# Performance work log

Hardware: AMD Instinct MI355X
Metric: run time of the kernel (lower is better)

The kernel has to match this reference:

```python
import jax, jax.numpy as jnp
import numpy as np

D_IN, H, L, B, ALPHA = 42, 800, 256, 16, 20
BOND_LENS = jnp.array([145.801, 152.326, 132.868], dtype=jnp.float32)  # N-CA, CA-C, C-N (pm)
BOND_ANGS = jnp.array([2.124, 1.941, 2.028], dtype=jnp.float32)


def setup_inputs() -> dict:
    key = jax.random.key(0)
    ks = jax.random.split(key, 10)
    s = 0.05
    return {
        "x": jax.random.normal(ks[0], (B, L, D_IN), dtype=jnp.float32),
        "w_ih_l0": jax.random.normal(ks[1], (2, 4 * H, D_IN), dtype=jnp.float32) * s,
        "w_hh_l0": jax.random.normal(ks[2], (2, 4 * H, H), dtype=jnp.float32) * s,
        "b_l0": jax.random.normal(ks[3], (2, 4 * H), dtype=jnp.float32) * s,
        "w_ih_l1": jax.random.normal(ks[4], (2, 4 * H, 2 * H), dtype=jnp.float32) * s,
        "w_hh_l1": jax.random.normal(ks[5], (2, 4 * H, H), dtype=jnp.float32) * s,
        "b_l1": jax.random.normal(ks[6], (2, 4 * H), dtype=jnp.float32) * s,
        "w_lin": jax.random.normal(ks[7], (ALPHA, 2 * H), dtype=jnp.float32) * s,
        "b_lin": jax.random.normal(ks[8], (ALPHA,), dtype=jnp.float32) * s,
        "alphabet": jax.random.uniform(ks[9], (ALPHA, 3), dtype=jnp.float32,
                                       minval=-np.pi, maxval=np.pi),
    }


def _lstm_dir(xs, w_ih, w_hh, b, reverse):
    # xs: (L, B, in) -> (L, B, H); PyTorch gate order i,f,g,o
    bsz = xs.shape[1]
    hdim = w_hh.shape[1]
    def step(carry, x_t):
        hp, cp = carry
        g = x_t @ w_ih.T + hp @ w_hh.T + b
        i, f, gg, o = jnp.split(g, 4, axis=-1)
        c = jax.nn.sigmoid(f) * cp + jax.nn.sigmoid(i) * jnp.tanh(gg)
        hn = jax.nn.sigmoid(o) * jnp.tanh(c)
        return (hn, c), hn
    init = (jnp.zeros((bsz, hdim), xs.dtype), jnp.zeros((bsz, hdim), xs.dtype))
    _, ys = jax.lax.scan(step, init, xs, reverse=reverse)
    return ys


def _bilstm_layer(xs, w_ih, w_hh, b):
    fwd = _lstm_dir(xs, w_ih[0], w_hh[0], b[0], reverse=False)
    bwd = _lstm_dir(xs, w_ih[1], w_hh[1], b[1], reverse=True)
    return jnp.concatenate([fwd, bwd], axis=-1)  # (L, B, 2H)


def _calculate_coordinates(torsions):
    # torsions: (L, B, 3) dihedrals -> NeRF backbone extension, (3 + 3L, B, 3)
    bsz = torsions.shape[1]
    A0 = jnp.broadcast_to(jnp.array([0., 0., 1.], jnp.float32), (bsz, 3))
    B0 = jnp.broadcast_to(jnp.array([0., 1., 0.], jnp.float32), (bsz, 3))
    C0 = jnp.broadcast_to(jnp.array([1., 0., 0.], jnp.float32), (bsz, 3))

    def step(carry, tors):
        A_, B_, C_ = carry
        outs = []
        for i in range(3):  # place N, CA, C of next residue
            T, R, P = BOND_ANGS[i], BOND_LENS[i], tors[:, i]
            D2 = jnp.stack([-R * jnp.cos(T) * jnp.ones_like(P),
                            R * jnp.cos(P) * jnp.sin(T),
                            R * jnp.sin(P) * jnp.sin(T)], axis=1)  # (B,3)
            bc = (C_ - B_) / jnp.linalg.norm(C_ - B_, axis=1, keepdims=True)
            Nv = jnp.cross(B_ - A_, bc)
            n = Nv / jnp.linalg.norm(Nv, axis=1, keepdims=True)
            M = jnp.stack([bc, jnp.cross(n, bc), n], axis=2)  # (B,3,3)
            D = jnp.einsum('bij,bj->bi', M, D2) + C_
            outs.append(D)
            A_, B_, C_ = B_, C_, D
        return (A_, B_, C_), jnp.stack(outs)  # (3, B, 3)

    _, new = jax.lax.scan(step, (A0, B0, C0), torsions)  # (L, 3, B, 3)
    init = jnp.stack([A0, B0, C0])  # (3, B, 3)
    return jnp.concatenate([init, new.reshape(-1, bsz, 3)], axis=0)


def reference(x, w_ih_l0, w_hh_l0, b_l0, w_ih_l1, w_hh_l1, b_l1, w_lin, b_lin, alphabet):
    xs = jnp.transpose(x, (1, 0, 2))  # (L, B, d_in), matches torch transpose(0,1)
    h1 = _bilstm_layer(xs, w_ih_l0, w_hh_l0, b_l0)
    h2 = _bilstm_layer(h1, w_ih_l1, w_hh_l1, b_l1)  # (L, B, 2H); eval mode: no dropout
    # Angularization: linear -> softmax over alphabet -> weighted dihedral lookup
    probs = jax.nn.softmax(h2 @ w_lin.T + b_lin, axis=-1)  # (L, B, ALPHA)
    sin_a, cos_a = jnp.sin(alphabet), jnp.cos(alphabet)     # (ALPHA, 3)
    ang = jnp.arctan2(probs @ sin_a, probs @ cos_a)         # (L, B, 3)
    return _calculate_coordinates(ang)
```

## Files before the change

kernel.cpp:

```cpp
#include <hip/hip_runtime.h>
#include <stdint.h>

typedef __attribute__((ext_vector_type(8))) short short8;
typedef __attribute__((ext_vector_type(4))) float floatx4;
typedef __attribute__((ext_vector_type(4))) unsigned int uintx4;

#define DEVINL __device__ __forceinline__

DEVINL unsigned short f2bf(float f) {
    unsigned int u = __float_as_uint(f);
    u += 0x7FFFu + ((u >> 16) & 1u);
    return (unsigned short)(u >> 16);
}
DEVINL float bf2f(unsigned short h) {
    return __uint_as_float(((unsigned int)h) << 16);
}
DEVINL float sigf(float x)     { return 1.0f / (1.0f + __expf(-x)); }
DEVINL float tanhfast(float x) { return 2.0f / (1.0f + __expf(-2.0f * x)) - 1.0f; }

constexpr int L_SEQ = 256, BATCH = 16, HID = 800, NGATE = 3200, DIN = 42, NALPHA = 20;
constexpr int HSLOT = BATCH * HID;
constexpr int NBLK_SCAN = 200;

constexpr size_t OFF_FLAGS   = 0;
constexpr size_t SZ_FLAGS    = 131072;
constexpr size_t SZ_WHH_L    = 10240000;
constexpr size_t OFF_WHH_HI  = SZ_FLAGS;
constexpr size_t OFF_WHH_LO  = OFF_WHH_HI + 2 * SZ_WHH_L;
constexpr size_t SZ_WIH1     = 20480000;
constexpr size_t OFF_WIH1_HI = OFF_WHH_LO + 2 * SZ_WHH_L;
constexpr size_t OFF_WIH1_LO = OFF_WIH1_HI + SZ_WIH1;
constexpr size_t OFF_PRE     = OFF_WIH1_LO + SZ_WIH1;
constexpr size_t SZ_PRE      = (size_t)2 * L_SEQ * BATCH * NGATE * 4;
constexpr size_t SZ_HP       = (size_t)257 * HSLOT * 4;
constexpr size_t OFF_H       = OFF_PRE + SZ_PRE;
constexpr size_t OFF_ANG     = OFF_H + 4 * SZ_HP;

__global__ __launch_bounds__(256) void pack_whh_kernel(
    const float* __restrict__ w0, const float* __restrict__ w1,
    unsigned short* __restrict__ hi, unsigned short* __restrict__ lo)
{
    size_t g = (size_t)blockIdx.x * 256 + threadIdx.x;
    if (g >= 1280000) return;
    int l = (int)(g & 63);
    size_t gg = g >> 6;
    int kk = (int)(gg % 25); gg /= 25;
    int nt = (int)(gg % 2);  gg /= 2;
    int jc = (int)(gg % 100); gg /= 100;
    int d  = (int)(gg % 2);
    int layer = (int)(gg / 2);
    const float* W = layer ? w1 : w0;
    int lr = nt * 16 + (l & 15);
    int gate = lr >> 3, jj = lr & 7;
    int r  = gate * 800 + jc * 8 + jj;
    int k0 = kk * 32 + (l >> 4) * 8;
    const float* s = W + ((size_t)d * NGATE + r) * HID + k0;
    short8 vh, vl;
    #pragma unroll
    for (int j = 0; j < 8; ++j) {
        float w = s[j];
        unsigned short h = f2bf(w);
        vh[j] = (short)h;
        vl[j] = (short)f2bf(w - bf2f(h));
    }
    size_t idx = (size_t)layer * 640000 + ((size_t)d * 100 + jc) * 3200
               + (size_t)(nt * 25 + kk) * 64 + l;
    ((short8*)hi)[idx] = vh;
    ((short8*)lo)[idx] = vl;
}

__global__ __launch_bounds__(256) void conv_wih1_kernel(
    const float* __restrict__ w, unsigned short* __restrict__ hi,
    unsigned short* __restrict__ lo)
{
    size_t g = (size_t)blockIdx.x * 256 + threadIdx.x;
    if (g >= 1280000) return;
    const float* s = w + g * 8;
    short8 vh, vl;
    #pragma unroll
    for (int j = 0; j < 8; ++j) {
        float x = s[j];
        unsigned short h = f2bf(x);
        vh[j] = (short)h;
        vl[j] = (short)f2bf(x - bf2f(h));
    }
    ((short8*)hi)[g] = vh;
    ((short8*)lo)[g] = vl;
}

__global__ __launch_bounds__(256) void pre0_kernel(
    const float* __restrict__ x, const float* __restrict__ wih0,
    const float* __restrict__ b0, float* __restrict__ pre0)
{
    int bid = blockIdx.x;
    int d = bid / 800; int rem = bid % 800;
    int rc = rem / 8, tc = rem % 8;
    int rbase = rc * 32, tbase = tc * 32;
    __shared__ float Wc[32][DIN];
    __shared__ float bias[32];
    __shared__ float xb[BATCH][DIN];
    int tid = threadIdx.x;
    for (int idx = tid; idx < 32 * DIN; idx += 256) {
        int rl = idx / DIN, k = idx % DIN;
        Wc[rl][k] = wih0[((size_t)d * NGATE + rbase + rl) * DIN + k];
    }
    if (tid < 32) bias[tid] = b0[d * NGATE + rbase + tid];
    __syncthreads();
    for (int tt = 0; tt < 32; ++tt) {
        int t = tbase + tt;
        for (int idx = tid; idx < BATCH * DIN; idx += 256) {
            int bb = idx / DIN, k = idx % DIN;
            xb[bb][k] = x[((size_t)bb * L_SEQ + t) * DIN + k];
        }
        __syncthreads();
        for (int o = tid; o < 512; o += 256) {
            int bb = o >> 5, rl = o & 31;
            float s = bias[rl];
            #pragma unroll 6
            for (int k = 0; k < DIN; ++k) s += xb[bb][k] * Wc[rl][k];
            pre0[((size_t)(d * L_SEQ + t) * BATCH + bb) * NGATE + rbase + rl] = s;
        }
        __syncthreads();
    }
}

DEVINL void batch_load_14(const uint32_t* base, uintx4* pk) {
    asm volatile(
        "global_load_dwordx4 %0, %14, off sc0 sc1\n\t"
        "global_load_dwordx4 %1, %14, off offset:16 sc0 sc1\n\t"
        "global_load_dwordx4 %2, %14, off offset:128 sc0 sc1\n\t"
        "global_load_dwordx4 %3, %14, off offset:144 sc0 sc1\n\t"
        "global_load_dwordx4 %4, %14, off offset:256 sc0 sc1\n\t"
        "global_load_dwordx4 %5, %14, off offset:272 sc0 sc1\n\t"
        "global_load_dwordx4 %6, %14, off offset:384 sc0 sc1\n\t"
        "global_load_dwordx4 %7, %14, off offset:400 sc0 sc1\n\t"
        "global_load_dwordx4 %8, %14, off offset:512 sc0 sc1\n\t"
        "global_load_dwordx4 %9, %14, off offset:528 sc0 sc1\n\t"
        "global_load_dwordx4 %10, %14, off offset:640 sc0 sc1\n\t"
        "global_load_dwordx4 %11, %14, off offset:656 sc0 sc1\n\t"
        "global_load_dwordx4 %12, %14, off offset:768 sc0 sc1\n\t"
        "global_load_dwordx4 %13, %14, off offset:784 sc0 sc1\n\t"
        "s_waitcnt vmcnt(0)"
        : "=&v"(pk[0]), "=&v"(pk[1]), "=&v"(pk[2]), "=&v"(pk[3]),
          "=&v"(pk[4]), "=&v"(pk[5]), "=&v"(pk[6]), "=&v"(pk[7]),
          "=&v"(pk[8]), "=&v"(pk[9]), "=&v"(pk[10]), "=&v"(pk[11]),
          "=&v"(pk[12]), "=&v"(pk[13])
        : "v"(base)
        : "memory");
}

DEVINL void batch_load_12(const uint32_t* base, uintx4* pk) {
    asm volatile(
        "global_load_dwordx4 %0, %12, off sc0 sc1\n\t"
        "global_load_dwordx4 %1, %12, off offset:16 sc0 sc1\n\t"
        "global_load_dwordx4 %2, %12, off offset:128 sc0 sc1\n\t"
        "global_load_dwordx4 %3, %12, off offset:144 sc0 sc1\n\t"
        "global_load_dwordx4 %4, %12, off offset:256 sc0 sc1\n\t"
        "global_load_dwordx4 %5, %12, off offset:272 sc0 sc1\n\t"
        "global_load_dwordx4 %6, %12, off offset:384 sc0 sc1\n\t"
        "global_load_dwordx4 %7, %12, off offset:400 sc0 sc1\n\t"
        "global_load_dwordx4 %8, %12, off offset:512 sc0 sc1\n\t"
        "global_load_dwordx4 %9, %12, off offset:528 sc0 sc1\n\t"
        "global_load_dwordx4 %10, %12, off offset:640 sc0 sc1\n\t"
        "global_load_dwordx4 %11, %12, off offset:656 sc0 sc1\n\t"
        "s_waitcnt vmcnt(0)"
        : "=&v"(pk[0]), "=&v"(pk[1]), "=&v"(pk[2]), "=&v"(pk[3]),
          "=&v"(pk[4]), "=&v"(pk[5]), "=&v"(pk[6]), "=&v"(pk[7]),
          "=&v"(pk[8]), "=&v"(pk[9]), "=&v"(pk[10]), "=&v"(pk[11])
        : "v"(base)
        : "memory");
}

DEVINL void unpack_u44(uintx4 p0, uintx4 p1, short8& ah, short8& al) {
    ah[0]=(short)(p0.x&0xffffu); al[0]=(short)(p0.x>>16);
    ah[1]=(short)(p0.y&0xffffu); al[1]=(short)(p0.y>>16);
    ah[2]=(short)(p0.z&0xffffu); al[2]=(short)(p0.z>>16);
    ah[3]=(short)(p0.w&0xffffu); al[3]=(short)(p0.w>>16);
    ah[4]=(short)(p1.x&0xffffu); al[4]=(short)(p1.x>>16);
    ah[5]=(short)(p1.y&0xffffu); al[5]=(short)(p1.y>>16);
    ah[6]=(short)(p1.z&0xffffu); al[6]=(short)(p1.z>>16);
    ah[7]=(short)(p1.w&0xffffu); al[7]=(short)(p1.w>>16);
}

template<int CNT, int KST>
DEVINL void mfma_k2(const uintx4* pk,
                    const short8* __restrict__ wH,
                    const short8* __restrict__ wL, int lane,
                    floatx4& out0, floatx4& out1)
{
    floatx4 p0 = {0.f,0.f,0.f,0.f}, q0 = {0.f,0.f,0.f,0.f};
    floatx4 p1 = {0.f,0.f,0.f,0.f}, q1 = {0.f,0.f,0.f,0.f};
    #pragma unroll
    for (int i = 0; i < CNT; ++i) {
        short8 ah, al;
        unpack_u44(pk[2 * i], pk[2 * i + 1], ah, al);
        int kk = KST + i;
        short8 bh0 = wH[(0 * 25 + kk) * 64 + lane];
        short8 bl0 = wL[(0 * 25 + kk) * 64 + lane];
        short8 bh1 = wH[(1 * 25 + kk) * 64 + lane];
        short8 bl1 = wL[(1 * 25 + kk) * 64 + lane];
        p0 = __builtin_amdgcn_mfma_f32_16x16x32_bf16(ah, bh0, p0, 0, 0, 0);
        q0 = __builtin_amdgcn_mfma_f32_16x16x32_bf16(ah, bl0, q0, 0, 0, 0);
        q0 = __builtin_amdgcn_mfma_f32_16x16x32_bf16(al, bh0, q0, 0, 0, 0);
        p1 = __builtin_amdgcn_mfma_f32_16x16x32_bf16(ah, bh1, p1, 0, 0, 0);
        q1 = __builtin_amdgcn_mfma_f32_16x16x32_bf16(ah, bl1, q1, 0, 0, 0);
        q1 = __builtin_amdgcn_mfma_f32_16x16x32_bf16(al, bh1, q1, 0, 0, 0);
    }
    out0 = p0 + q0;
    out1 = p1 + q1;
}

__global__ __launch_bounds__(256, 1) void scan_kernel(
    const unsigned short* __restrict__ wpackH,
    const unsigned short* __restrict__ wpackL,
    const float* __restrict__ pre,
    uint32_t* hFP, uint32_t* hBP)
{
    __shared__ __align__(16) unsigned short wldsH[25600];
    __shared__ __align__(16) unsigned short wldsL[25600];
    __shared__ __align__(16) float exch[2][2][4][64][4];
    __shared__ float cbuf[128];
    int tid = threadIdx.x;
    int bid = blockIdx.x;
    int d = bid / 100, jc = bid % 100;

    {
        const short8* sh = (const short8*)wpackH + ((size_t)d * 100 + jc) * 3200;
        const short8* sl = (const short8*)wpackL + ((size_t)d * 100 + jc) * 3200;
        short8* dh = (short8*)wldsH;
        short8* dl = (short8*)wldsL;
        for (int i = tid; i < 3200; i += 256) { dh[i] = sh[i]; dl[i] = sl[i]; }
    }
    if (tid < 128) cbuf[tid] = 0.0f;
    __syncthreads();

    int lane = tid & 63, w = tid >> 6;
    int st = 6 * w + (w > 0 ? 1 : 0);
    int bA = lane & 15, q = lane >> 4;
    int fb = (tid >> 3) & 15, fj = tid & 7;

    uint32_t* hOutP = d ? hBP : hFP;
    const uint32_t* hInP = d ? hBP : hFP;
    const short8* wH8 = (const short8*)wldsH;
    const short8* wL8 = (const short8*)wldsL;

    int npoll = (w == 0) ? 28 : 24;
    int jcBase = (w == 0) ? 0 : (4 + 24 * w);
    int jx = jcBase + ((lane < npoll) ? lane : 0);
    size_t pofs = (size_t)(jx & 15) * HID + (size_t)jx * 8;

    for (int s = 0; s < L_SEQ; ++s) {
        int t = d ? (L_SEQ - 1 - s) : s;
        int islot = d ? (t + 1) : t;
        const uint32_t* slotBase = hInP + (size_t)islot * HSLOT;
        const uint32_t* base = slotBase + bA * HID + st * 32 + q * 8;

        float pv[4];
        if (tid < 128) {
            const float* pp = pre + ((size_t)(d * L_SEQ + t) * BATCH + fb) * NGATE
                            + jc * 8 + fj;
            #pragma unroll
            for (int gate = 0; gate < 4; ++gate) pv[gate] = pp[gate * 800];
        }

        {
            const uint32_t* pw = slotBase + pofs;
            for (;;) {
                uint32_t v = __hip_atomic_load(pw, __ATOMIC_RELAXED,
                                               __HIP_MEMORY_SCOPE_AGENT);
                if (__all(lane >= npoll || v != 0xFFFFFFFFu)) break;
                __builtin_amdgcn_s_sleep(2);
            }
        }

        uintx4 pk[14];
        floatx4 acc0, acc1;
        for (;;) {
            if (w == 0) {
                batch_load_14(base, pk);
                mfma_k2<7, 0 >(pk, wH8, wL8, lane, acc0, acc1);
            } else if (w == 1) {
                batch_load_12(base, pk);
                mfma_k2<6, 7 >(pk, wH8, wL8, lane, acc0, acc1);
            } else if (w == 2) {
                batch_load_12(base, pk);
                mfma_k2<6, 13>(pk, wH8, wL8, lane, acc0, acc1);
            } else {
                batch_load_12(base, pk);
                mfma_k2<6, 19>(pk, wH8, wL8, lane, acc0, acc1);
            }
            bool bad = (acc0[0] != acc0[0]) || (acc0[1] != acc0[1])
                     || (acc0[2] != acc0[2]) || (acc0[3] != acc0[3])
                     || (acc1[0] != acc1[0]) || (acc1[1] != acc1[1])
                     || (acc1[2] != acc1[2]) || (acc1[3] != acc1[3]);
            if (!__any(bad)) break;
        }

        int p = s & 1;
        *(floatx4*)&exch[p][0][w][lane][0] = acc0;
        *(floatx4*)&exch[p][1][w][lane][0] = acc1;
        __syncthreads();

        if (tid < 128) {
            float G[4];
            #pragma unroll
            for (int gate = 0; gate < 4; ++gate) {
                int lr = gate * 8 + fj;
                int nt2 = lr >> 4, n = lr & 15;
                int ln = ((fb >> 2) << 4) | n;
                int rg = fb & 3;
                G[gate] = pv[gate]
                        + exch[p][nt2][0][ln][rg] + exch[p][nt2][1][ln][rg]
                        + exch[p][nt2][2][ln][rg] + exch[p][nt2][3][ln][rg];
            }
            float i_ = sigf(G[0]), f_ = sigf(G[1]);
            float g_ = tanhfast(G[2]), o_ = sigf(G[3]);
            float c = f_ * cbuf[tid] + i_ * g_;
            cbuf[tid] = c;
            float h = o_ * tanhfast(c);
            int oslot = d ? t : (t + 1);
            size_t oidx = (size_t)oslot * HSLOT + fb * HID + jc * 8 + fj;
            unsigned short hh = f2bf(h);
            uint32_t pko = (uint32_t)hh
                         | ((uint32_t)f2bf(h - bf2f(hh)) << 16);
            __hip_atomic_store(&hOutP[oidx], pko, __ATOMIC_RELAXED,
                               __HIP_MEMORY_SCOPE_AGENT);
        }
    }
}

__global__ __launch_bounds__(256, 1) void gemm_pre1_kernel(
    const uint32_t* __restrict__ hFP, const uint32_t* __restrict__ hBP,
    const unsigned short* __restrict__ wih1H, const unsigned short* __restrict__ wih1L,
    const float* __restrict__ b1, float* __restrict__ pre1)
{
    int bid = blockIdx.x;
    int d = bid / 3200; int rst = bid % 3200;
    int mblk = rst / 50, nblk = rst % 50;
    __shared__ __align__(16) unsigned short AslH[64][40];
    __shared__ __align__(16) unsigned short AslL[64][40];
    __shared__ __align__(16) unsigned short BslH[64][40];
    __shared__ __align__(16) unsigned short BslL[64][40];
    int tid = threadIdx.x, lane = tid & 63, w = tid >> 6;
    int wm = w >> 1, wn = w & 1;
    floatx4 acc[2][2] = {};
    int row = tid >> 2, ch = tid & 3;
    int m_row = mblk * 64 + row;
    int t = m_row >> 4, bb = m_row & 15;
    int la = lane & 15, q8 = (lane >> 4) * 8;

    for (int kk = 0; kk < 50; ++kk) {
        int k0 = kk * 32 + ch * 8;
        size_t aoff = (kk < 25)
            ? ((size_t)(t + 1) * HSLOT + bb * HID + k0)
            : ((size_t)t * HSLOT + bb * HID + (k0 - 800));
        const uint32_t* ap = ((kk < 25) ? hFP : hBP) + aoff;
        uint4 p0 = *(const uint4*)ap;
        uint4 p1 = *(const uint4*)(ap + 4);
        short8 ah, al;
        ah[0]=(short)(p0.x&0xffffu); al[0]=(short)(p0.x>>16);
        ah[1]=(short)(p0.y&0xffffu); al[1]=(short)(p0.y>>16);
        ah[2]=(short)(p0.z&0xffffu); al[2]=(short)(p0.z>>16);
        ah[3]=(short)(p0.w&0xffffu); al[3]=(short)(p0.w>>16);
        ah[4]=(short)(p1.x&0xffffu); al[4]=(short)(p1.x>>16);
        ah[5]=(short)(p1.y&0xffffu); al[5]=(short)(p1.y>>16);
        ah[6]=(short)(p1.z&0xffffu); al[6]=(short)(p1.z>>16);
        ah[7]=(short)(p1.w&0xffffu); al[7]=(short)(p1.w>>16);
        *(short8*)&AslH[row][ch * 8] = ah;
        *(short8*)&AslL[row][ch * 8] = al;
        size_t boff = ((size_t)d * NGATE + nblk * 64 + row) * 1600 + kk * 32 + ch * 8;
        *(short8*)&BslH[row][ch * 8] = *(const short8*)(wih1H + boff);
        *(short8*)&BslL[row][ch * 8] = *(const short8*)(wih1L + boff);
        __syncthreads();
        #pragma unroll
        for (int ms = 0; ms < 2; ++ms) {
            short8 fah = *(const short8*)&AslH[wm * 32 + ms * 16 + la][q8];
            short8 fal = *(const short8*)&AslL[wm * 32 + ms * 16 + la][q8];
            #pragma unroll
            for (int ns = 0; ns < 2; ++ns) {
                short8 fbh = *(const short8*)&BslH[wn * 32 + ns * 16 + la][q8];
                short8 fbl = *(const short8*)&BslL[wn * 32 + ns * 16 + la][q8];
                acc[ms][ns] = __builtin_amdgcn_mfma_f32_16x16x32_bf16(fah, fbh, acc[ms][ns], 0, 0, 0);
                acc[ms][ns] = __builtin_amdgcn_mfma_f32_16x16x32_bf16(fah, fbl, acc[ms][ns], 0, 0, 0);
                acc[ms][ns] = __builtin_amdgcn_mfma_f32_16x16x32_bf16(fal, fbh, acc[ms][ns], 0, 0, 0);
            }
        }
        __syncthreads();
    }
    #pragma unroll
    for (int ms = 0; ms < 2; ++ms)
        #pragma unroll
        for (int ns = 0; ns < 2; ++ns)
            #pragma unroll
            for (int rg = 0; rg < 4; ++rg) {
                int m = mblk * 64 + wm * 32 + ms * 16 + (lane >> 4) * 4 + rg;
                int t2 = m >> 4, b2 = m & 15;
                int r = nblk * 64 + wn * 32 + ns * 16 + (lane & 15);
                float val = acc[ms][ns][rg] + b1[d * NGATE + r];
                pre1[((size_t)(d * L_SEQ + t2) * BATCH + b2) * NGATE + r] = val;
            }
}

__global__ __launch_bounds__(256) void head_kernel(
    const uint32_t* __restrict__ h2FP, const uint32_t* __restrict__ h2BP,
    const float* __restrict__ wlin, const float* __restrict__ blin,
    const float* __restrict__ alphabet, float* __restrict__ ang)
{
    int t = blockIdx.x, tid = threadIdx.x;
    __shared__ float lg[BATCH * NALPHA];
    __shared__ float probs[BATCH * NALPHA];
    for (int i = tid; i < BATCH * NALPHA; i += 256) {
        int a = i % NALPHA, b = i / NALPHA;
        size_t fo = (size_t)(t + 1) * HSLOT + b * HID;
        size_t bo = (size_t)t * HSLOT + b * HID;
        const float* wa = wlin + (size_t)a * 1600;
        float s = blin[a];
        #pragma unroll 4
        for (int k = 0; k < HID; ++k) {
            uint32_t uf = h2FP[fo + k], ub = h2BP[bo + k];
            float hf = bf2f((unsigned short)uf) + bf2f((unsigned short)(uf >> 16));
            float hb = bf2f((unsigned short)ub) + bf2f((unsigned short)(ub >> 16));
            s += hf * wa[k] + hb * wa[800 + k];
        }
        lg[b * NALPHA + a] = s;
    }
    __syncthreads();
    if (tid < BATCH) {
        int b = tid;
        float mx = -1e30f;
        for (int a = 0; a < NALPHA; ++a) mx = fmaxf(mx, lg[b * NALPHA + a]);
        float sum = 0.f;
        for (int a = 0; a < NALPHA; ++a) {
            float e = __expf(lg[b * NALPHA + a] - mx);
            probs[b * NALPHA + a] = e; sum += e;
        }
        float inv = 1.0f / sum;
        for (int a = 0; a < NALPHA; ++a) probs[b * NALPHA + a] *= inv;
    }
    __syncthreads();
    if (tid < BATCH * 3) {
        int b = tid / 3, i = tid % 3;
        float ss = 0.f, cc = 0.f;
        for (int a = 0; a < NALPHA; ++a) {
            float al = alphabet[a * 3 + i], p = probs[b * NALPHA + a];
            ss += p * sinf(al); cc += p * cosf(al);
        }
        ang[((size_t)t * BATCH + b) * 3 + i] = atan2f(ss, cc);
    }
}

__global__ __launch_bounds__(64) void coords_kernel(
    const float* __restrict__ ang, float* __restrict__ out)
{
    int b = threadIdx.x;
    if (b >= BATCH) return;
    const float LENS[3] = {145.801f, 152.326f, 132.868f};
    const float ANGS[3] = {2.124f, 1.941f, 2.028f};
    float Ax = 0.f, Ay = 0.f, Az = 1.f;
    float Bx = 0.f, By = 1.f, Bz = 0.f;
    float Cx = 1.f, Cy = 0.f, Cz = 0.f;
    out[((size_t)0 * BATCH + b) * 3 + 0] = 0.f; out[((size_t)0 * BATCH + b) * 3 + 1] = 0.f; out[((size_t)0 * BATCH + b) * 3 + 2] = 1.f;
    out[((size_t)1 * BATCH + b) * 3 + 0] = 0.f; out[((size_t)1 * BATCH + b) * 3 + 1] = 1.f; out[((size_t)1 * BATCH + b) * 3 + 2] = 0.f;
    out[((size_t)2 * BATCH + b) * 3 + 0] = 1.f; out[((size_t)2 * BATCH + b) * 3 + 1] = 0.f; out[((size_t)2 * BATCH + b) * 3 + 2] = 0.f;
    for (int t = 0; t < L_SEQ; ++t) {
        #pragma unroll
        for (int i = 0; i < 3; ++i) {
            float P = ang[((size_t)t * BATCH + b) * 3 + i];
            float R = LENS[i], T = ANGS[i];
            float sT = sinf(T);
            float D2x = -R * cosf(T);
            float D2y = R * cosf(P) * sT;
            float D2z = R * sinf(P) * sT;
            float bx = Cx - Bx, by = Cy - By, bz = Cz - Bz;
            float binv = 1.0f / sqrtf(bx * bx + by * by + bz * bz);
            bx *= binv; by *= binv; bz *= binv;
            float ux = Bx - Ax, uy = By - Ay, uz = Bz - Az;
            float nx = uy * bz - uz * by;
            float ny = uz * bx - ux * bz;
            float nz = ux * by - uy * bx;
            float ninv = 1.0f / sqrtf(nx * nx + ny * ny + nz * nz);
            nx *= ninv; ny *= ninv; nz *= ninv;
            float cxx = ny * bz - nz * by;
            float cxy = nz * bx - nx * bz;
            float cxz = nx * by - ny * bx;
            float Dx = bx * D2x + cxx * D2y + nx * D2z + Cx;
            float Dy = by * D2x + cxy * D2y + ny * D2z + Cy;
            float Dz = bz * D2x + cxz * D2y + nz * D2z + Cz;
            size_t orow = 3 + (size_t)t * 3 + i;
            out[(orow * BATCH + b) * 3 + 0] = Dx;
            out[(orow * BATCH + b) * 3 + 1] = Dy;
            out[(orow * BATCH + b) * 3 + 2] = Dz;
            Ax = Bx; Ay = By; Az = Bz;
            Bx = Cx; By = Cy; Bz = Cz;
            Cx = Dx; Cy = Dy; Cz = Dz;
        }
    }
}

extern "C" void kernel_launch(void* const* d_in, const int* in_sizes, int n_in,
                              void* d_out, int out_size, void* d_ws, size_t ws_size,
                              hipStream_t stream)
{
    const float* x       = (const float*)d_in[0];
    const float* w_ih_l0 = (const float*)d_in[1];
    const float* w_hh_l0 = (const float*)d_in[2];
    const float* b_l0    = (const float*)d_in[3];
    const float* w_ih_l1 = (const float*)d_in[4];
    const float* w_hh_l1 = (const float*)d_in[5];
    const float* b_l1    = (const float*)d_in[6];
    const float* w_lin   = (const float*)d_in[7];
    const float* b_lin   = (const float*)d_in[8];
    const float* alphabet= (const float*)d_in[9];
    (void)in_sizes; (void)n_in; (void)out_size; (void)ws_size;

    char* ws = (char*)d_ws;
    unsigned short* whhHi   = (unsigned short*)(ws + OFF_WHH_HI);
    unsigned short* whhLo   = (unsigned short*)(ws + OFF_WHH_LO);
    unsigned short* wih1Hi  = (unsigned short*)(ws + OFF_WIH1_HI);
    unsigned short* wih1Lo  = (unsigned short*)(ws + OFF_WIH1_LO);
    float*          pre     = (float*)(ws + OFF_PRE);
    uint32_t*       hFP     = (uint32_t*)(ws + OFF_H + 0 * SZ_HP);
    uint32_t*       hBP     = (uint32_t*)(ws + OFF_H + 1 * SZ_HP);
    uint32_t*       h2FP    = (uint32_t*)(ws + OFF_H + 2 * SZ_HP);
    uint32_t*       h2BP    = (uint32_t*)(ws + OFF_H + 3 * SZ_HP);
    float*          angbuf  = (float*)(ws + OFF_ANG);

    const size_t slotB = (size_t)HSLOT * 4;
    hipMemsetAsync(ws + OFF_H, 0xFF, 4 * SZ_HP, stream);
    hipMemsetAsync((char*)hFP, 0, slotB, stream);
    hipMemsetAsync((char*)hBP + 256 * slotB, 0, slotB, stream);
    hipMemsetAsync((char*)h2FP, 0, slotB, stream);
    hipMemsetAsync((char*)h2BP + 256 * slotB, 0, slotB, stream);

    pack_whh_kernel<<<5000, 256, 0, stream>>>(w_hh_l0, w_hh_l1, whhHi, whhLo);
    conv_wih1_kernel<<<5000, 256, 0, stream>>>(w_ih_l1, wih1Hi, wih1Lo);
    pre0_kernel<<<1600, 256, 0, stream>>>(x, w_ih_l0, b_l0, pre);

    scan_kernel<<<NBLK_SCAN, 256, 0, stream>>>(whhHi, whhLo, pre, hFP, hBP);
    gemm_pre1_kernel<<<6400, 256, 0, stream>>>(hFP, hBP, wih1Hi, wih1Lo, b_l1, pre);
    constexpr size_t LOFF = SZ_WHH_L / 2;
    scan_kernel<<<NBLK_SCAN, 256, 0, stream>>>(whhHi + LOFF, whhLo + LOFF, pre,
                                               h2FP, h2BP);

    head_kernel<<<L_SEQ, 256, 0, stream>>>(h2FP, h2BP, w_lin, b_lin, alphabet, angbuf);
    coords_kernel<<<1, 64, 0, stream>>>(angbuf, (float*)d_out);
}
```

Before: 3.516 ms.

## Enlarge layer-1 input GEMM tiles with prefetch; check sentinels before MFMA in scan

The layer-1 input-projection GEMM moves from 64x64 to 128x128 tiles, so each wave now owns a 4x4 MFMA sub-tile. It stages the packed hi/lo A operand once in shared memory and register-prefetches the next K slice while computing the current one, which cuts global reloads and launch count. The scan kernel now checks raw loaded values for the 0xFFFFFFFF sentinel and retries only the load, instead of running the MFMAs and testing the results for NaN, which avoids wasted matrix work on stale data. The coordinates kernel hoists the constant sin/cos terms and uses fast intrinsics and rsqrt, at some cost in precision.

```diff
diff --git a/kernel.cpp b/kernel.cpp
--- a/kernel.cpp
+++ b/kernel.cpp
@@ -182,6 +182,16 @@
     ah[7]=(short)(p1.w&0xffffu); al[7]=(short)(p1.w>>16);
 }
 
+template<int CNT>
+DEVINL bool sentinel_in(const uintx4* pk) {
+    bool bad = false;
+    #pragma unroll
+    for (int i = 0; i < 2 * CNT; ++i)
+        bad = bad || (pk[i].x == 0xFFFFFFFFu) || (pk[i].y == 0xFFFFFFFFu)
+                  || (pk[i].z == 0xFFFFFFFFu) || (pk[i].w == 0xFFFFFFFFu);
+    return __any(bad);
+}
+
 template<int CNT, int KST>
 DEVINL void mfma_k2(const uintx4* pk,
                     const short8* __restrict__ wH,
@@ -275,25 +285,34 @@
 
         uintx4 pk[14];
         floatx4 acc0, acc1;
-        for (;;) {
-            if (w == 0) {
+        if (w == 0) {
+            for (;;) {
                 batch_load_14(base, pk);
-                mfma_k2<7, 0 >(pk, wH8, wL8, lane, acc0, acc1);
-            } else if (w == 1) {
+                if (!sentinel_in<7>(pk)) break;
+                __builtin_amdgcn_s_sleep(1);
+            }
+            mfma_k2<7, 0 >(pk, wH8, wL8, lane, acc0, acc1);
+        } else if (w == 1) {
+            for (;;) {
                 batch_load_12(base, pk);
-                mfma_k2<6, 7 >(pk, wH8, wL8, lane, acc0, acc1);
-            } else if (w == 2) {
+                if (!sentinel_in<6>(pk)) break;
+                __builtin_amdgcn_s_sleep(1);
+            }
+            mfma_k2<6, 7 >(pk, wH8, wL8, lane, acc0, acc1);
+        } else if (w == 2) {
+            for (;;) {
                 batch_load_12(base, pk);
-                mfma_k2<6, 13>(pk, wH8, wL8, lane, acc0, acc1);
-            } else {
+                if (!sentinel_in<6>(pk)) break;
+                __builtin_amdgcn_s_sleep(1);
+            }
+            mfma_k2<6, 13>(pk, wH8, wL8, lane, acc0, acc1);
+        } else {
+            for (;;) {
                 batch_load_12(base, pk);
-                mfma_k2<6, 19>(pk, wH8, wL8, lane, acc0, acc1);
-            }
-            bool bad = (acc0[0] != acc0[0]) || (acc0[1] != acc0[1])
-                     || (acc0[2] != acc0[2]) || (acc0[3] != acc0[3])
-                     || (acc1[0] != acc1[0]) || (acc1[1] != acc1[1])
-                     || (acc1[2] != acc1[2]) || (acc1[3] != acc1[3]);
-            if (!__any(bad)) break;
+                if (!sentinel_in<6>(pk)) break;
+                __builtin_amdgcn_s_sleep(1);
+            }
+            mfma_k2<6, 19>(pk, wH8, wL8, lane, acc0, acc1);
         }
 
         int p = s & 1;
@@ -335,67 +354,74 @@
     const float* __restrict__ b1, float* __restrict__ pre1)
 {
     int bid = blockIdx.x;
-    int d = bid / 3200; int rst = bid % 3200;
-    int mblk = rst / 50, nblk = rst % 50;
-    __shared__ __align__(16) unsigned short AslH[64][40];
-    __shared__ __align__(16) unsigned short AslL[64][40];
-    __shared__ __align__(16) unsigned short BslH[64][40];
-    __shared__ __align__(16) unsigned short BslL[64][40];
+    int d = bid / 800; int rst = bid % 800;
+    int mblk = rst / 25, nblk = rst % 25;
+    __shared__ __align__(16) uint32_t       Au[128][36];
+    __shared__ __align__(16) unsigned short BH[128][40];
+    __shared__ __align__(16) unsigned short BL[128][40];
     int tid = threadIdx.x, lane = tid & 63, w = tid >> 6;
     int wm = w >> 1, wn = w & 1;
-    floatx4 acc[2][2] = {};
-    int row = tid >> 2, ch = tid & 3;
-    int m_row = mblk * 64 + row;
+    floatx4 acc[4][4] = {};
+    int row = tid >> 1, half = tid & 1;
+    int m_row = mblk * 128 + row;
     int t = m_row >> 4, bb = m_row & 15;
-    int la = lane & 15, q8 = (lane >> 4) * 8;
-
-    for (int kk = 0; kk < 50; ++kk) {
-        int k0 = kk * 32 + ch * 8;
+    int la = lane & 15, q = lane >> 4, q8 = q * 8;
+
+    uintx4 ra[4];
+    short8 rbh[2], rbl[2];
+
+    auto LOAD = [&](int kk) {
+        int k0 = kk * 32 + half * 16;
         size_t aoff = (kk < 25)
             ? ((size_t)(t + 1) * HSLOT + bb * HID + k0)
             : ((size_t)t * HSLOT + bb * HID + (k0 - 800));
-        const uint32_t* ap = ((kk < 25) ? hFP : hBP) + aoff;
-        uint4 p0 = *(const uint4*)ap;
-        uint4 p1 = *(const uint4*)(ap + 4);
-        short8 ah, al;
-        ah[0]=(short)(p0.x&0xffffu); al[0]=(short)(p0.x>>16);
-        ah[1]=(short)(p0.y&0xffffu); al[1]=(short)(p0.y>>16);
-        ah[2]=(short)(p0.z&0xffffu); al[2]=(short)(p0.z>>16);
-        ah[3]=(short)(p0.w&0xffffu); al[3]=(short)(p0.w>>16);
-        ah[4]=(short)(p1.x&0xffffu); al[4]=(short)(p1.x>>16);
-        ah[5]=(short)(p1.y&0xffffu); al[5]=(short)(p1.y>>16);
-        ah[6]=(short)(p1.z&0xffffu); al[6]=(short)(p1.z>>16);
-        ah[7]=(short)(p1.w&0xffffu); al[7]=(short)(p1.w>>16);
-        *(short8*)&AslH[row][ch * 8] = ah;
-        *(short8*)&AslL[row][ch * 8] = al;
-        size_t boff = ((size_t)d * NGATE + nblk * 64 + row) * 1600 + kk * 32 + ch * 8;
-        *(short8*)&BslH[row][ch * 8] = *(const short8*)(wih1H + boff);
-        *(short8*)&BslL[row][ch * 8] = *(const short8*)(wih1L + boff);
+        const uintx4* ap = (const uintx4*)(((kk < 25) ? hFP : hBP) + aoff);
+        ra[0] = ap[0]; ra[1] = ap[1]; ra[2] = ap[2]; ra[3] = ap[3];
+        size_t boff = ((size_t)d * NGATE + nblk * 128 + row) * 1600
+                    + (size_t)kk * 32 + half * 16;
+        const short8* bh = (const short8*)(wih1H + boff);
+        const short8* bl = (const short8*)(wih1L + boff);
+        rbh[0] = bh[0]; rbh[1] = bh[1];
+        rbl[0] = bl[0]; rbl[1] = bl[1];
+    };
+
+    LOAD(0);
+    for (int kk = 0; kk < 50; ++kk) {
+        {
+            uintx4* da = (uintx4*)&Au[row][half * 16];
+            da[0] = ra[0]; da[1] = ra[1]; da[2] = ra[2]; da[3] = ra[3];
+            short8* dh = (short8*)&BH[row][half * 16];
+            dh[0] = rbh[0]; dh[1] = rbh[1];
+            short8* dl = (short8*)&BL[row][half * 16];
+            dl[0] = rbl[0]; dl[1] = rbl[1];
+        }
         __syncthreads();
+        if (kk < 49) LOAD(kk + 1);
         #pragma unroll
-        for (int ms = 0; ms < 2; ++ms) {
-            short8 fah = *(const short8*)&AslH[wm * 32 + ms * 16 + la][q8];
-            short8 fal = *(const short8*)&AslL[wm * 32 + ms * 16 + la][q8];
+        for (int ms = 0; ms < 4; ++ms) {
+            const uintx4* pa = (const uintx4*)&Au[wm * 64 + ms * 16 + la][q8];
+            short8 ah, al;
+            unpack_u44(pa[0], pa[1], ah, al);
             #pragma unroll
-            for (int ns = 0; ns < 2; ++ns) {
-                short8 fbh = *(const short8*)&BslH[wn * 32 + ns * 16 + la][q8];
-                short8 fbl = *(const short8*)&BslL[wn * 32 + ns * 16 + la][q8];
-                acc[ms][ns] = __builtin_amdgcn_mfma_f32_16x16x32_bf16(fah, fbh, acc[ms][ns], 0, 0, 0);
-                acc[ms][ns] = __builtin_amdgcn_mfma_f32_16x16x32_bf16(fah, fbl, acc[ms][ns], 0, 0, 0);
-                acc[ms][ns] = __builtin_amdgcn_mfma_f32_16x16x32_bf16(fal, fbh, acc[ms][ns], 0, 0, 0);
+            for (int ns = 0; ns < 4; ++ns) {
+                short8 fbh = *(const short8*)&BH[wn * 64 + ns * 16 + la][q8];
+                short8 fbl = *(const short8*)&BL[wn * 64 + ns * 16 + la][q8];
+                acc[ms][ns] = __builtin_amdgcn_mfma_f32_16x16x32_bf16(ah, fbh, acc[ms][ns], 0, 0, 0);
+                acc[ms][ns] = __builtin_amdgcn_mfma_f32_16x16x32_bf16(ah, fbl, acc[ms][ns], 0, 0, 0);
+                acc[ms][ns] = __builtin_amdgcn_mfma_f32_16x16x32_bf16(al, fbh, acc[ms][ns], 0, 0, 0);
             }
         }
         __syncthreads();
     }
     #pragma unroll
-    for (int ms = 0; ms < 2; ++ms)
+    for (int ms = 0; ms < 4; ++ms)
         #pragma unroll
-        for (int ns = 0; ns < 2; ++ns)
+        for (int ns = 0; ns < 4; ++ns)
             #pragma unroll
             for (int rg = 0; rg < 4; ++rg) {
-                int m = mblk * 64 + wm * 32 + ms * 16 + (lane >> 4) * 4 + rg;
+                int m = mblk * 128 + wm * 64 + ms * 16 + q * 4 + rg;
                 int t2 = m >> 4, b2 = m & 15;
-                int r = nblk * 64 + wn * 32 + ns * 16 + (lane & 15);
+                int r = nblk * 128 + wn * 64 + ns * 16 + la;
                 float val = acc[ms][ns][rg] + b1[d * NGATE + r];
                 pre1[((size_t)(d * L_SEQ + t2) * BATCH + b2) * NGATE + r] = val;
             }
@@ -456,6 +482,9 @@
     if (b >= BATCH) return;
     const float LENS[3] = {145.801f, 152.326f, 132.868f};
     const float ANGS[3] = {2.124f, 1.941f, 2.028f};
+    float sT[3], cT[3];
+    #pragma unroll
+    for (int i = 0; i < 3; ++i) { sT[i] = sinf(ANGS[i]); cT[i] = cosf(ANGS[i]); }
     float Ax = 0.f, Ay = 0.f, Az = 1.f;
     float Bx = 0.f, By = 1.f, Bz = 0.f;
     float Cx = 1.f, Cy = 0.f, Cz = 0.f;
@@ -466,19 +495,19 @@
         #pragma unroll
         for (int i = 0; i < 3; ++i) {
             float P = ang[((size_t)t * BATCH + b) * 3 + i];
-            float R = LENS[i], T = ANGS[i];
-            float sT = sinf(T);
-            float D2x = -R * cosf(T);
-            float D2y = R * cosf(P) * sT;
-            float D2z = R * sinf(P) * sT;
+            float R = LENS[i];
+            float sP = __sinf(P), cP = __cosf(P);
+            float D2x = -R * cT[i];
+            float D2y = R * cP * sT[i];
+            float D2z = R * sP * sT[i];
             float bx = Cx - Bx, by = Cy - By, bz = Cz - Bz;
-            float binv = 1.0f / sqrtf(bx * bx + by * by + bz * bz);
+            float binv = rsqrtf(bx * bx + by * by + bz * bz);
             bx *= binv; by *= binv; bz *= binv;
             float ux = Bx - Ax, uy = By - Ay, uz = Bz - Az;
             float nx = uy * bz - uz * by;
             float ny = uz * bx - ux * bz;
             float nz = ux * by - uy * bx;
-            float ninv = 1.0f / sqrtf(nx * nx + ny * ny + nz * nz);
+            float ninv = rsqrtf(nx * nx + ny * ny + nz * nz);
             nx *= ninv; ny *= ninv; nz *= ninv;
             float cxx = ny * bz - nz * by;
             float cxy = nz * bx - nx * bz;
@@ -526,18 +555,18 @@
     float*          angbuf  = (float*)(ws + OFF_ANG);
 
     const size_t slotB = (size_t)HSLOT * 4;
-    hipMemsetAsync(ws + OFF_H, 0xFF, 4 * SZ_HP, stream);
-    hipMemsetAsync((char*)hFP, 0, slotB, stream);
-    hipMemsetAsync((char*)hBP + 256 * slotB, 0, slotB, stream);
-    hipMemsetAsync((char*)h2FP, 0, slotB, stream);
-    hipMemsetAsync((char*)h2BP + 256 * slotB, 0, slotB, stream);
+    (void)hipMemsetAsync(ws + OFF_H, 0xFF, 4 * SZ_HP, stream);
+    (void)hipMemsetAsync((char*)hFP, 0, slotB, stream);
+    (void)hipMemsetAsync((char*)hBP + 256 * slotB, 0, slotB, stream);
+    (void)hipMemsetAsync((char*)h2FP, 0, slotB, stream);
+    (void)hipMemsetAsync((char*)h2BP + 256 * slotB, 0, slotB, stream);
 
     pack_whh_kernel<<<5000, 256, 0, stream>>>(w_hh_l0, w_hh_l1, whhHi, whhLo);
     conv_wih1_kernel<<<5000, 256, 0, stream>>>(w_ih_l1, wih1Hi, wih1Lo);
     pre0_kernel<<<1600, 256, 0, stream>>>(x, w_ih_l0, b_l0, pre);
 
     scan_kernel<<<NBLK_SCAN, 256, 0, stream>>>(whhHi, whhLo, pre, hFP, hBP);
-    gemm_pre1_kernel<<<6400, 256, 0, stream>>>(hFP, hBP, wih1Hi, wih1Lo, b_l1, pre);
+    gemm_pre1_kernel<<<1600, 256, 0, stream>>>(hFP, hBP, wih1Hi, wih1Lo, b_l1, pre);
     constexpr size_t LOFF = SZ_WHH_L / 2;
     scan_kernel<<<NBLK_SCAN, 256, 0, stream>>>(whhHi + LOFF, whhLo + LOFF, pre,
                                                h2FP, h2BP);
```

Measured after the change: 3.360 ms. -4.4%, faster.
